# Performance work log

Measured on AMD Instinct MI355X. Metric: run time of the kernel, lower is better.

## Reference

```python
import jax, jax.numpy as jnp
import numpy as np

B, N, D = 8, 2048, 512

def setup_inputs() -> dict:
    key = jax.random.key(0)
    ks = jax.random.split(key, 8)
    s = 1.0 / np.sqrt(D)
    return {
        "inputs": jax.random.normal(ks[0], (B, N, D), dtype=jnp.float32),
        "mask": jnp.ones((B, N), dtype=jnp.int32),
        "Wk": jax.random.normal(ks[1], (D, D), dtype=jnp.float32) * s,
        "bk": jax.random.normal(ks[2], (D,), dtype=jnp.float32) * s,
        "Wq": jax.random.normal(ks[3], (D, D), dtype=jnp.float32) * s,
        "bq": jax.random.normal(ks[4], (D,), dtype=jnp.float32) * s,
        "Wv": jax.random.normal(ks[5], (D, D), dtype=jnp.float32) * s,
        "bv": jax.random.normal(ks[6], (D,), dtype=jnp.float32) * s,
    }

def reference(inputs, mask, Wk, bk, Wq, bq, Wv, bv):
    # torch Linear: y = x @ W.T + b
    keys = jnp.einsum('bnd,ed->bne', inputs, Wk) + bk
    queries = jnp.einsum('bnd,ed->bne', inputs, Wq) + bq
    values = jnp.einsum('bnd,ed->bne', inputs, Wv) + bv
    norm = jnp.sqrt(jnp.asarray(D, inputs.dtype))
    scores = jnp.einsum('bqd,bkd->bqk', queries, keys) / norm  # [B,N,N]
    scores = jnp.where(mask[:, None, :] == 0, jnp.asarray(-1e9, scores.dtype), scores)
    attn = jax.nn.softmax(scores, axis=-1)
    return jnp.einsum('bqk,bkd->bqd', attn, values)
```

## Files before the change

### kernel.cpp

```cpp
#include <hip/hip_runtime.h>
#include <hip/hip_bf16.h>


typedef __attribute__((ext_vector_type(8))) short short8;
typedef __attribute__((ext_vector_type(4))) float f32x4;

#define DEV __device__ __forceinline__
#define GLOBAL_AS __attribute__((address_space(1)))
#define LDS_AS __attribute__((address_space(3)))

static DEV ushort f2bs(float f) {
  union { float f; unsigned u; } x; x.f = f;
  unsigned r = (x.u + 0x7fffu + ((x.u >> 16) & 1u)) >> 16;
  return (ushort)r;
}

static DEV f32x4 mfma16(short8 a, short8 b, f32x4 c) {
  return __builtin_amdgcn_mfma_f32_16x16x32_bf16(a, b, c, 0, 0, 0);
}

static DEV void async16(const void* g, void* l) {
  __builtin_amdgcn_global_load_lds((const GLOBAL_AS void*)g, (LDS_AS void*)l, 16, 0, 0);
}

__global__ void convert_all(const float* __restrict__ wq, const float* __restrict__ wk,
                            const float* __restrict__ wv, const float* __restrict__ x,
                            ushort* __restrict__ wb, ushort* __restrict__ xb,
                            float* __restrict__ lde) {
  int i = blockIdx.x * 256 + threadIdx.x;
  if (i >= 2293760) {
    int off = (i - 2293760) * 4;
    float4 z; z.x = 0.f; z.y = 0.f; z.z = 0.f; z.w = 0.f;
    *(float4*)(lde + off) = z;
    return;
  }
  const float* src;
  ushort* dst;
  if (i < 196608) {
    int which = i >> 16;
    int off = (i & 65535) * 4;
    src = ((which == 0) ? wq : (which == 1) ? wk : wv) + off;
    dst = wb + (size_t)which * 262144 + off;
  } else {
    int off = (i - 196608) * 4;
    src = x + off;
    dst = xb + off;
  }
  float4 v = *(const float4*)src;
  ushort4 o;
  o.x = f2bs(v.x); o.y = f2bs(v.y); o.z = f2bs(v.z); o.w = f2bs(v.w);
  *(ushort4*)dst = o;
}

#define PH_ST_A(pp, kt, rd)                                                    \
  do {                                                                         \
    int rowbase_ = (rd) * 64 + wave * 8;                                       \
    int r_ = rowbase_ + (lane >> 3);                                           \
    int gc_ = (lane & 7) ^ (r_ & 7);                                           \
    async16(gA + (size_t)(arow0 + r_) * glda + (kt) * 64 + gc_ * 8,            \
            SdA + (pp) * 16384 + rowbase_ * 64);                               \
  } while (0)

#define PH_ST_B(pp, kt, rd)                                                    \
  do {                                                                         \
    int rowbase_ = (rd) * 64 + wave * 8;                                       \
    int r_ = rowbase_ + (lane >> 3);                                           \
    int gc_ = (lane & 7) ^ (r_ & 7);                                           \
    async16(gB + (size_t)(brow0 + r_) * gldb + (kt) * 64 + gc_ * 8,            \
            SdB + (pp) * 8192 + rowbase_ * 64);                                \
  } while (0)

#define PH_READ(pp, ks, afx, bfx)                                              \
  do {                                                                         \
    const ushort* Ap_ = SdA + (pp) * 16384;                                    \
    const ushort* Bp_ = SdB + (pp) * 8192;                                     \
    _Pragma("unroll")                                                          \
    for (int mf = 0; mf < 4; mf++) {                                           \
      int ra = wm * 64 + mf * 16 + c16;                                        \
      afx[mf] = *(const short8*)&Ap_[ra * 64 + ((((ks)*4 + quad) ^ (ra & 7)) * 8)]; \
    }                                                                          \
    _Pragma("unroll")                                                          \
    for (int nf = 0; nf < 4; nf++) {                                           \
      int rb = wn * 64 + nf * 16 + c16;                                        \
      bfx[nf] = *(const short8*)&Bp_[rb * 64 + ((((ks)*4 + quad) ^ (rb & 7)) * 8)]; \
    }                                                                          \
  } while (0)

#define PH_MFMA(afx, bfx, h)                                                   \
  do {                                                                         \
    __builtin_amdgcn_s_setprio(1);                                             \
    _Pragma("unroll")                                                          \
    for (int mf = (h) * 2; mf < (h) * 2 + 2; mf++)                             \
      _Pragma("unroll")                                                        \
      for (int nf = 0; nf < 4; nf++)                                           \
        acc[mf][nf] = mfma16(afx[mf], bfx[nf], acc[mf][nf]);                   \
    __builtin_amdgcn_s_setprio(0);                                             \
  } while (0)

#define PH_TILE(pp, kt, dostage)                                               \
  do {                                                                         \
    PH_READ(pp, 0, af0, bf0);                                                  \
    __builtin_amdgcn_s_barrier();                                              \
    asm volatile("s_waitcnt lgkmcnt(0)" ::: "memory");                         \
    __builtin_amdgcn_sched_barrier(0);                                         \
    PH_MFMA(af0, bf0, 0);                                                      \
    __builtin_amdgcn_s_barrier();                                              \
    PH_READ(pp, 1, af1, bf1);                                                  \
    __builtin_amdgcn_s_barrier();                                              \
    asm volatile("s_waitcnt lgkmcnt(0)" ::: "memory");                         \
    __builtin_amdgcn_sched_barrier(0);                                         \
    PH_MFMA(af0, bf0, 1);                                                      \
    __builtin_amdgcn_s_barrier();         \
    if (dostage) { PH_ST_A(pp, (kt) + 2, 0); PH_ST_A(pp, (kt) + 2, 1);         \
                   PH_ST_A(pp, (kt) + 2, 2); }                                 \
    PH_MFMA(af1, bf1, 0);                                                      \
    __builtin_amdgcn_s_barrier();                                              \
    if (dostage) { PH_ST_A(pp, (kt) + 2, 3); PH_ST_B(pp, (kt) + 2, 0);         \
                   PH_ST_B(pp, (kt) + 2, 1); }                                 \
    PH_MFMA(af1, bf1, 1);                                                      \
    if (dostage) { asm volatile("s_waitcnt vmcnt(6)" ::: "memory"); }          \
    else         { asm volatile("s_waitcnt vmcnt(0)" ::: "memory"); }          \
    __builtin_amdgcn_sched_barrier(0);                                         \
    __builtin_amdgcn_s_barrier();        \
  } while (0)

#define PH_PROLOGUE()                                                          \
  do {                                                                         \
    PH_ST_A(0, 0, 0); PH_ST_A(0, 0, 1); PH_ST_A(0, 0, 2); PH_ST_A(0, 0, 3);    \
    PH_ST_B(0, 0, 0); PH_ST_B(0, 0, 1);                                        \
    PH_ST_A(1, 1, 0); PH_ST_A(1, 1, 1); PH_ST_A(1, 1, 2); PH_ST_A(1, 1, 3);    \
    PH_ST_B(1, 1, 0); PH_ST_B(1, 1, 1);                                        \
    asm volatile("s_waitcnt vmcnt(6)" ::: "memory");                           \
    __builtin_amdgcn_sched_barrier(0);                                         \
    __builtin_amdgcn_s_barrier();                                              \
  } while (0)

__launch_bounds__(512, 2)
__global__ void qkv_gemm(const ushort* __restrict__ Xb, const ushort* __restrict__ Wb,
                         const float* __restrict__ bq, const float* __restrict__ bk,
                         const float* __restrict__ bv,
                         ushort* __restrict__ Qb, ushort* __restrict__ Kb,
                         ushort* __restrict__ Vtb) {
  const int rowblk = blockIdx.x;
  const int colblk = blockIdx.y;
  const int z = colblk >> 2;

  extern __shared__ ushort Sd[];
  ushort* SdA = Sd;
  ushort* SdB = Sd + 32768;

  const int tid = threadIdx.x;
  const int wave = tid >> 6, lane = tid & 63, quad = lane >> 4, c16 = lane & 15;
  const int wm = wave >> 1, wn = wave & 1;

  const ushort* gA = Xb;  const int glda = 512; const int arow0 = rowblk * 256;
  const ushort* gB = Wb;  const int gldb = 512; const int brow0 = colblk * 128;

  f32x4 acc[4][4];
#pragma unroll
  for (int mf = 0; mf < 4; mf++)
#pragma unroll
    for (int nf = 0; nf < 4; nf++) acc[mf][nf] = (f32x4)0.0f;

  PH_PROLOGUE();
  short8 af0[4], bf0[4], af1[4], bf1[4];
  for (int i = 0; i < 4; i++) {
    const int ds = (i < 3);
    PH_TILE(0, 2 * i, ds);
    PH_TILE(1, 2 * i + 1, ds);
  }

  const float* bias = (z == 0) ? bq : (z == 1) ? bk : bv;
  const int col0 = (colblk & 3) * 128 + wn * 64;
  float bvals[4];
#pragma unroll
  for (int nf = 0; nf < 4; nf++) bvals[nf] = bias[col0 + nf * 16 + c16];
  const float sc = (z == 0) ? 0.044194173824159216f : 1.0f;

  const int row0 = rowblk * 256 + wm * 64;
  if (z < 2) {
    ushort* O = (z == 0) ? Qb : Kb;
#pragma unroll
    for (int mf = 0; mf < 4; mf++)
#pragma unroll
      for (int nf = 0; nf < 4; nf++) {
        int el = col0 + nf * 16 + c16;
#pragma unroll
        for (int r = 0; r < 4; r++) {
          int n = row0 + mf * 16 + quad * 4 + r;
          O[(size_t)n * 512 + el] = f2bs((acc[mf][nf][r] + bvals[nf]) * sc);
        }
      }
  } else {
    __syncthreads();
    ushort* T = Sd;
#pragma unroll
    for (int nf = 0; nf < 4; nf++) {
      int ell = wn * 64 + nf * 16 + c16;
#pragma unroll
      for (int mf = 0; mf < 4; mf++) {
        int n0 = wm * 64 + mf * 16 + quad * 4;
        ushort4 o;
        o.x = f2bs(acc[mf][nf][0] + bvals[nf]);
        o.y = f2bs(acc[mf][nf][1] + bvals[nf]);
        o.z = f2bs(acc[mf][nf][2] + bvals[nf]);
        o.w = f2bs(acc[mf][nf][3] + bvals[nf]);
        *(ushort4*)&T[ell * 256 + (((n0 >> 3) ^ (ell & 31)) << 3) + (n0 & 4)] = o;
      }
    }
    __syncthreads();
    const int b = rowblk >> 3;
    const int nbase = (rowblk & 7) * 256;
    const int elbase = (colblk & 3) * 128;
    const int c4 = tid & 3, er = tid >> 2;
    size_t ge = ((size_t)b * 512 + elbase + er) * 2048;
#pragma unroll
    for (int j = 0; j < 8; j++) {
      int ch = j * 4 + c4;
      short8 v = *(short8*)&T[er * 256 + ((ch ^ (er & 31)) << 3)];
      *(short8*)(Vtb + ge + nbase + ch * 8) = v;
    }
  }
}

__launch_bounds__(512, 2)
__global__ void gemm_s(const ushort* __restrict__ Kb, const ushort* __restrict__ Qb,
                       const int* __restrict__ mask, ushort* __restrict__ Pm,
                       float* __restrict__ l) {
  const int bid = blockIdx.x;
  const int b = bid & 7;
  const int rowblk = (bid >> 3) & 7;
  const int colblk = bid >> 6;

  extern __shared__ ushort Sd[];
  ushort* SdA = Sd;
  ushort* SdB = Sd + 32768;

  const int tid = threadIdx.x;
  const int wave = tid >> 6, lane = tid & 63, quad = lane >> 4, c16 = lane & 15;
  const int wm = wave >> 1, wn = wave & 1;

  const ushort* gA = Kb + (size_t)b * 2048 * 512;  const int glda = 512;
  const int arow0 = rowblk * 256;
  const ushort* gB = Qb + (size_t)b * 2048 * 512;  const int gldb = 512;
  const int brow0 = colblk * 128;

  f32x4 acc[4][4];
#pragma unroll
  for (int mf = 0; mf < 4; mf++)
#pragma unroll
    for (int nf = 0; nf < 4; nf++) acc[mf][nf] = (f32x4)0.0f;

  PH_PROLOGUE();
  short8 af0[4], bf0[4], af1[4], bf1[4];
  for (int i = 0; i < 4; i++) {
    const int ds = (i < 3);
    PH_TILE(0, 2 * i, ds);
    PH_TILE(1, 2 * i + 1, ds);
  }

  float lpart[4] = {0.0f, 0.0f, 0.0f, 0.0f};
  __syncthreads();
  ushort* T = Sd;
#pragma unroll
  for (int mf = 0; mf < 4; mf++) {
    int keyl = wm * 64 + mf * 16 + quad * 4;
    int4 mv = *(const int4*)&mask[b * 2048 + rowblk * 256 + keyl];
    float m0 = mv.x ? 1.0f : 0.0f, m1 = mv.y ? 1.0f : 0.0f;
    float m2 = mv.z ? 1.0f : 0.0f, m3 = mv.w ? 1.0f : 0.0f;
#pragma unroll
    for (int nf = 0; nf < 4; nf++) {
      int ql = wn * 64 + nf * 16 + c16;
      float p0 = __expf(acc[mf][nf][0]) * m0;
      float p1 = __expf(acc[mf][nf][1]) * m1;
      float p2 = __expf(acc[mf][nf][2]) * m2;
      float p3 = __expf(acc[mf][nf][3]) * m3;
      ushort4 o;
      o.x = f2bs(p0); o.y = f2bs(p1); o.z = f2bs(p2); o.w = f2bs(p3);
      *(ushort4*)&T[ql * 256 + (((keyl >> 3) ^ (ql & 31)) << 3) + (keyl & 4)] = o;
      lpart[nf] += p0 + p1 + p2 + p3;
    }
  }
#pragma unroll
  for (int nf = 0; nf < 4; nf++) {
    float v = lpart[nf];
    v += __shfl_xor(v, 16, 64);
    v += __shfl_xor(v, 32, 64);
    if (quad == 0)
      atomicAdd(&l[b * 2048 + colblk * 128 + wn * 64 + nf * 16 + c16], v);
  }
  __syncthreads();
  {
    const int c4 = tid & 3, er = tid >> 2;
    size_t gq = ((size_t)b * 2048 + colblk * 128 + er) * 2048;
#pragma unroll
    for (int j = 0; j < 8; j++) {
      int ch = j * 4 + c4;
      short8 v = *(short8*)&T[er * 256 + ((ch ^ (er & 31)) << 3)];
      *(short8*)(Pm + gq + rowblk * 256 + ch * 8) = v;
    }
  }
}

__launch_bounds__(512, 2)
__global__ void gemm_o(const ushort* __restrict__ Pm, const ushort* __restrict__ Vtb,
                       const float* __restrict__ l, float* __restrict__ out) {
  const int bid = blockIdx.x;
  const int b = bid & 7;
  const int rowblk = (bid >> 3) & 7;
  const int colblk = bid >> 6;

  extern __shared__ ushort Sd[];
  ushort* SdA = Sd;
  ushort* SdB = Sd + 32768;

  const int tid = threadIdx.x;
  const int wave = tid >> 6, lane = tid & 63, quad = lane >> 4, c16 = lane & 15;
  const int wm = wave >> 1, wn = wave & 1;

  const ushort* gA = Pm + (size_t)b * 2048 * 2048;  const int glda = 2048;
  const int arow0 = rowblk * 256;
  const ushort* gB = Vtb + (size_t)b * 512 * 2048;  const int gldb = 2048;
  const int brow0 = colblk * 128;

  f32x4 acc[4][4];
#pragma unroll
  for (int mf = 0; mf < 4; mf++)
#pragma unroll
    for (int nf = 0; nf < 4; nf++) acc[mf][nf] = (f32x4)0.0f;

  PH_PROLOGUE();
  short8 af0[4], bf0[4], af1[4], bf1[4];
  for (int i = 0; i < 16; i++) {
    const int ds = (i < 15);
    PH_TILE(0, 2 * i, ds);
    PH_TILE(1, 2 * i + 1, ds);
  }

  const int row0 = rowblk * 256 + wm * 64;
  const int col0 = colblk * 128 + wn * 64;
  float linv[4][4];
#pragma unroll
  for (int mf = 0; mf < 4; mf++)
#pragma unroll
    for (int r = 0; r < 4; r++)
      linv[mf][r] = 1.0f / l[b * 2048 + row0 + mf * 16 + quad * 4 + r];
#pragma unroll
  for (int mf = 0; mf < 4; mf++)
#pragma unroll
    for (int nf = 0; nf < 4; nf++) {
      int col = col0 + nf * 16 + c16;
#pragma unroll
      for (int r = 0; r < 4; r++) {
        int row = row0 + mf * 16 + quad * 4 + r;
        out[((size_t)b * 2048 + row) * 512 + col] = acc[mf][nf][r] * linv[mf][r];
      }
    }
}

extern "C" void kernel_launch(void* const* d_in, const int* in_sizes, int n_in,
                              void* d_out, int out_size, void* d_ws, size_t ws_size,
                              hipStream_t stream) {
  (void)in_sizes; (void)n_in; (void)out_size; (void)ws_size;
  const float* X    = (const float*)d_in[0];
  const int*   mask = (const int*)d_in[1];
  const float* Wk   = (const float*)d_in[2];
  const float* bk   = (const float*)d_in[3];
  const float* Wq   = (const float*)d_in[4];
  const float* bq   = (const float*)d_in[5];
  const float* Wv   = (const float*)d_in[6];
  const float* bv   = (const float*)d_in[7];
  float* out = (float*)d_out;

  ushort* ws  = (ushort*)d_ws;
  ushort* Pm  = ws;
  ushort* Xb  = ws;
  ushort* Wb  = ws + (size_t)33554432;
  ushort* Qb  = Wb + (size_t)786432;
  ushort* Kb  = Qb + (size_t)8388608;
  ushort* Vtb = Kb + (size_t)8388608;
  float*  lde = (float*)(Vtb + (size_t)8388608);

  convert_all<<<8976, 256, 0, stream>>>(Wq, Wk, Wv, X, Wb, Xb, lde);
  qkv_gemm<<<dim3(64, 12), 512, 98304, stream>>>(Xb, Wb, bq, bk, bv, Qb, Kb, Vtb);
  gemm_s<<<1024, 512, 98304, stream>>>(Kb, Qb, mask, Pm, lde);
  gemm_o<<<256, 512, 98304, stream>>>(Pm, Vtb, lde, out);
}
```

Before: 218.8 us.

## Use single-buffered LDS GEMM loop in qkv and score kernels for higher occupancy

Replaces the double-buffered async-LDS pipelined mainloop in qkv_gemm and gemm_s with a simple single-buffer load/sync/compute step, halving LDS to 48KB and raising launch bounds to 4 blocks per CU. The transpose epilogues are split into two passes so they fit the smaller LDS. gemm_s also moves to a 3D grid with batch in z, which changes block scheduling order. The aim is to hide latency through more resident blocks instead of software pipelining. The cost is losing load/compute overlap within a block and adding barriers, and register pressure under the tighter launch bound may cause spills.

```diff
diff --git a/kernel.cpp b/kernel.cpp
--- a/kernel.cpp
+++ b/kernel.cpp
@@ -50,6 +50,216 @@
   ushort4 o;
   o.x = f2bs(v.x); o.y = f2bs(v.y); o.z = f2bs(v.z); o.w = f2bs(v.w);
   *(ushort4*)dst = o;
+}
+
+#define ST_A1(kt, rd)                                                          \
+  do {                                                                         \
+    int rowbase_ = (rd) * 64 + wave * 8;                                       \
+    int r_ = rowbase_ + (lane >> 3);                                           \
+    int gc_ = (lane & 7) ^ (r_ & 7);                                           \
+    async16(gA + (size_t)(arow0 + r_) * glda + (kt) * 64 + gc_ * 8,            \
+            SdA + rowbase_ * 64);                                              \
+  } while (0)
+
+#define ST_B1(kt, rd)                                                          \
+  do {                                                                         \
+    int rowbase_ = (rd) * 64 + wave * 8;                                       \
+    int r_ = rowbase_ + (lane >> 3);                                           \
+    int gc_ = (lane & 7) ^ (r_ & 7);                                           \
+    async16(gB + (size_t)(brow0 + r_) * gldb + (kt) * 64 + gc_ * 8,            \
+            SdB + rowbase_ * 64);                                              \
+  } while (0)
+
+#define SIMPLE_STEP(kt)                                                        \
+  do {                                                                         \
+    __syncthreads();                                                           \
+    ST_A1(kt, 0); ST_A1(kt, 1); ST_A1(kt, 2); ST_A1(kt, 3);                    \
+    ST_B1(kt, 0); ST_B1(kt, 1);                                                \
+    __syncthreads();                                                           \
+    _Pragma("unroll")                                                          \
+    for (int ks = 0; ks < 2; ks++) {                                           \
+      short8 af[4], bf[4];                                                     \
+      _Pragma("unroll")                                                        \
+      for (int mf = 0; mf < 4; mf++) {                                         \
+        int ra = wm * 64 + mf * 16 + c16;                                      \
+        af[mf] = *(const short8*)&SdA[ra * 64 + (((ks * 4 + quad) ^ (ra & 7)) * 8)]; \
+      }                                                                        \
+      _Pragma("unroll")                                                        \
+      for (int nf = 0; nf < 4; nf++) {                                         \
+        int rb = wn * 64 + nf * 16 + c16;                                      \
+        bf[nf] = *(const short8*)&SdB[rb * 64 + (((ks * 4 + quad) ^ (rb & 7)) * 8)]; \
+      }                                                                        \
+      _Pragma("unroll")                                                        \
+      for (int mf = 0; mf < 4; mf++)                                           \
+        _Pragma("unroll")                                                      \
+        for (int nf = 0; nf < 4; nf++)                                         \
+          acc[mf][nf] = mfma16(af[mf], bf[nf], acc[mf][nf]);                   \
+    }                                                                          \
+  } while (0)
+
+__launch_bounds__(512, 4)
+__global__ void qkv_gemm(const ushort* __restrict__ Xb, const ushort* __restrict__ Wb,
+                         const float* __restrict__ bq, const float* __restrict__ bk,
+                         const float* __restrict__ bv,
+                         ushort* __restrict__ Qb, ushort* __restrict__ Kb,
+                         ushort* __restrict__ Vtb) {
+  const int rowblk = blockIdx.x;
+  const int colblk = blockIdx.y;
+  const int z = colblk >> 2;
+
+  extern __shared__ ushort Sd[];
+  ushort* SdA = Sd;
+  ushort* SdB = Sd + 16384;
+
+  const int tid = threadIdx.x;
+  const int wave = tid >> 6, lane = tid & 63, quad = lane >> 4, c16 = lane & 15;
+  const int wm = wave >> 1, wn = wave & 1;
+
+  const ushort* gA = Xb;  const int glda = 512; const int arow0 = rowblk * 256;
+  const ushort* gB = Wb;  const int gldb = 512; const int brow0 = colblk * 128;
+
+  f32x4 acc[4][4];
+#pragma unroll
+  for (int mf = 0; mf < 4; mf++)
+#pragma unroll
+    for (int nf = 0; nf < 4; nf++) acc[mf][nf] = (f32x4)0.0f;
+
+  for (int kt = 0; kt < 8; kt++) SIMPLE_STEP(kt);
+
+  const float* bias = (z == 0) ? bq : (z == 1) ? bk : bv;
+  const int col0 = (colblk & 3) * 128 + wn * 64;
+  float bvals[4];
+#pragma unroll
+  for (int nf = 0; nf < 4; nf++) bvals[nf] = bias[col0 + nf * 16 + c16];
+  const float sc = (z == 0) ? 0.044194173824159216f : 1.0f;
+
+  const int row0 = rowblk * 256 + wm * 64;
+  if (z < 2) {
+    ushort* O = (z == 0) ? Qb : Kb;
+#pragma unroll
+    for (int mf = 0; mf < 4; mf++)
+#pragma unroll
+      for (int nf = 0; nf < 4; nf++) {
+        int el = col0 + nf * 16 + c16;
+#pragma unroll
+        for (int r = 0; r < 4; r++) {
+          int n = row0 + mf * 16 + quad * 4 + r;
+          O[(size_t)n * 512 + el] = f2bs((acc[mf][nf][r] + bvals[nf]) * sc);
+        }
+      }
+  } else {
+    ushort* T = Sd;
+    const int bb = rowblk >> 3;
+    const int nbase = (rowblk & 7) * 256;
+    const int elbase = (colblk & 3) * 128;
+    const int c4 = tid & 3, er = tid >> 2;
+    __syncthreads();
+#pragma unroll
+    for (int pass = 0; pass < 2; pass++) {
+      if ((wm >> 1) == pass) {
+#pragma unroll
+        for (int nf = 0; nf < 4; nf++) {
+          int ell = wn * 64 + nf * 16 + c16;
+#pragma unroll
+          for (int mf = 0; mf < 4; mf++) {
+            int n0p = (wm & 1) * 64 + mf * 16 + quad * 4;
+            ushort4 o;
+            o.x = f2bs(acc[mf][nf][0] + bvals[nf]);
+            o.y = f2bs(acc[mf][nf][1] + bvals[nf]);
+            o.z = f2bs(acc[mf][nf][2] + bvals[nf]);
+            o.w = f2bs(acc[mf][nf][3] + bvals[nf]);
+            *(ushort4*)&T[ell * 128 + (((n0p >> 3) ^ (ell & 15)) << 3) + (n0p & 4)] = o;
+          }
+        }
+      }
+      __syncthreads();
+      size_t ge = ((size_t)bb * 512 + elbase + er) * 2048;
+#pragma unroll
+      for (int j = 0; j < 4; j++) {
+        int ch = j * 4 + c4;
+        short8 v = *(short8*)&T[er * 128 + ((ch ^ (er & 15)) << 3)];
+        *(short8*)(Vtb + ge + nbase + pass * 128 + ch * 8) = v;
+      }
+      __syncthreads();
+    }
+  }
+}
+
+__launch_bounds__(512, 4)
+__global__ void gemm_s(const ushort* __restrict__ Kb, const ushort* __restrict__ Qb,
+                       const int* __restrict__ mask, ushort* __restrict__ Pm,
+                       float* __restrict__ l) {
+  const int b = blockIdx.z;
+  const int rowblk = blockIdx.x;
+  const int colblk = blockIdx.y;
+
+  extern __shared__ ushort Sd[];
+  ushort* SdA = Sd;
+  ushort* SdB = Sd + 16384;
+
+  const int tid = threadIdx.x;
+  const int wave = tid >> 6, lane = tid & 63, quad = lane >> 4, c16 = lane & 15;
+  const int wm = wave >> 1, wn = wave & 1;
+
+  const ushort* gA = Kb + (size_t)b * 2048 * 512;  const int glda = 512;
+  const int arow0 = rowblk * 256;
+  const ushort* gB = Qb + (size_t)b * 2048 * 512;  const int gldb = 512;
+  const int brow0 = colblk * 128;
+
+  f32x4 acc[4][4];
+#pragma unroll
+  for (int mf = 0; mf < 4; mf++)
+#pragma unroll
+    for (int nf = 0; nf < 4; nf++) acc[mf][nf] = (f32x4)0.0f;
+
+  for (int kt = 0; kt < 8; kt++) SIMPLE_STEP(kt);
+
+  float lpart[4] = {0.0f, 0.0f, 0.0f, 0.0f};
+  ushort* T = Sd;
+  const int c4 = tid & 3, er = tid >> 2;
+  __syncthreads();
+#pragma unroll
+  for (int pass = 0; pass < 2; pass++) {
+    if ((wm >> 1) == pass) {
+#pragma unroll
+      for (int mf = 0; mf < 4; mf++) {
+        int k0p = (wm & 1) * 64 + mf * 16 + quad * 4;
+        int keyg = rowblk * 256 + pass * 128 + k0p;
+        int4 mv = *(const int4*)&mask[b * 2048 + keyg];
+        float m0 = mv.x ? 1.0f : 0.0f, m1 = mv.y ? 1.0f : 0.0f;
+        float m2 = mv.z ? 1.0f : 0.0f, m3 = mv.w ? 1.0f : 0.0f;
+#pragma unroll
+        for (int nf = 0; nf < 4; nf++) {
+          int ql = wn * 64 + nf * 16 + c16;
+          float p0 = __expf(acc[mf][nf][0]) * m0;
+          float p1 = __expf(acc[mf][nf][1]) * m1;
+          float p2 = __expf(acc[mf][nf][2]) * m2;
+          float p3 = __expf(acc[mf][nf][3]) * m3;
+          ushort4 o;
+          o.x = f2bs(p0); o.y = f2bs(p1); o.z = f2bs(p2); o.w = f2bs(p3);
+          *(ushort4*)&T[ql * 128 + (((k0p >> 3) ^ (ql & 15)) << 3) + (k0p & 4)] = o;
+          lpart[nf] += p0 + p1 + p2 + p3;
+        }
+      }
+    }
+    __syncthreads();
+    size_t gq = ((size_t)b * 2048 + colblk * 128 + er) * 2048;
+#pragma unroll
+    for (int j = 0; j < 4; j++) {
+      int ch = j * 4 + c4;
+      short8 v = *(short8*)&T[er * 128 + ((ch ^ (er & 15)) << 3)];
+      *(short8*)(Pm + gq + rowblk * 256 + pass * 128 + ch * 8) = v;
+    }
+    __syncthreads();
+  }
+#pragma unroll
+  for (int nf = 0; nf < 4; nf++) {
+    float v = lpart[nf];
+    v += __shfl_xor(v, 16, 64);
+    v += __shfl_xor(v, 32, 64);
+    if (quad == 0)
+      atomicAdd(&l[b * 2048 + colblk * 128 + wn * 64 + nf * 16 + c16], v);
+  }
 }
 
 #define PH_ST_A(pp, kt, rd)                                                    \
@@ -136,173 +346,6 @@
   } while (0)
 
 __launch_bounds__(512, 2)
-__global__ void qkv_gemm(const ushort* __restrict__ Xb, const ushort* __restrict__ Wb,
-                         const float* __restrict__ bq, const float* __restrict__ bk,
-                         const float* __restrict__ bv,
-                         ushort* __restrict__ Qb, ushort* __restrict__ Kb,
-                         ushort* __restrict__ Vtb) {
-  const int rowblk = blockIdx.x;
-  const int colblk = blockIdx.y;
-  const int z = colblk >> 2;
-
-  extern __shared__ ushort Sd[];
-  ushort* SdA = Sd;
-  ushort* SdB = Sd + 32768;
-
-  const int tid = threadIdx.x;
-  const int wave = tid >> 6, lane = tid & 63, quad = lane >> 4, c16 = lane & 15;
-  const int wm = wave >> 1, wn = wave & 1;
-
-  const ushort* gA = Xb;  const int glda = 512; const int arow0 = rowblk * 256;
-  const ushort* gB = Wb;  const int gldb = 512; const int brow0 = colblk * 128;
-
-  f32x4 acc[4][4];
-#pragma unroll
-  for (int mf = 0; mf < 4; mf++)
-#pragma unroll
-    for (int nf = 0; nf < 4; nf++) acc[mf][nf] = (f32x4)0.0f;
-
-  PH_PROLOGUE();
-  short8 af0[4], bf0[4], af1[4], bf1[4];
-  for (int i = 0; i < 4; i++) {
-    const int ds = (i < 3);
-    PH_TILE(0, 2 * i, ds);
-    PH_TILE(1, 2 * i + 1, ds);
-  }
-
-  const float* bias = (z == 0) ? bq : (z == 1) ? bk : bv;
-  const int col0 = (colblk & 3) * 128 + wn * 64;
-  float bvals[4];
-#pragma unroll
-  for (int nf = 0; nf < 4; nf++) bvals[nf] = bias[col0 + nf * 16 + c16];
-  const float sc = (z == 0) ? 0.044194173824159216f : 1.0f;
-
-  const int row0 = rowblk * 256 + wm * 64;
-  if (z < 2) {
-    ushort* O = (z == 0) ? Qb : Kb;
-#pragma unroll
-    for (int mf = 0; mf < 4; mf++)
-#pragma unroll
-      for (int nf = 0; nf < 4; nf++) {
-        int el = col0 + nf * 16 + c16;
-#pragma unroll
-        for (int r = 0; r < 4; r++) {
-          int n = row0 + mf * 16 + quad * 4 + r;
-          O[(size_t)n * 512 + el] = f2bs((acc[mf][nf][r] + bvals[nf]) * sc);
-        }
-      }
-  } else {
-    __syncthreads();
-    ushort* T = Sd;
-#pragma unroll
-    for (int nf = 0; nf < 4; nf++) {
-      int ell = wn * 64 + nf * 16 + c16;
-#pragma unroll
-      for (int mf = 0; mf < 4; mf++) {
-        int n0 = wm * 64 + mf * 16 + quad * 4;
-        ushort4 o;
-        o.x = f2bs(acc[mf][nf][0] + bvals[nf]);
-        o.y = f2bs(acc[mf][nf][1] + bvals[nf]);
-        o.z = f2bs(acc[mf][nf][2] + bvals[nf]);
-        o.w = f2bs(acc[mf][nf][3] + bvals[nf]);
-        *(ushort4*)&T[ell * 256 + (((n0 >> 3) ^ (ell & 31)) << 3) + (n0 & 4)] = o;
-      }
-    }
-    __syncthreads();
-    const int b = rowblk >> 3;
-    const int nbase = (rowblk & 7) * 256;
-    const int elbase = (colblk & 3) * 128;
-    const int c4 = tid & 3, er = tid >> 2;
-    size_t ge = ((size_t)b * 512 + elbase + er) * 2048;
-#pragma unroll
-    for (int j = 0; j < 8; j++) {
-      int ch = j * 4 + c4;
-      short8 v = *(short8*)&T[er * 256 + ((ch ^ (er & 31)) << 3)];
-      *(short8*)(Vtb + ge + nbase + ch * 8) = v;
-    }
-  }
-}
-
-__launch_bounds__(512, 2)
-__global__ void gemm_s(const ushort* __restrict__ Kb, const ushort* __restrict__ Qb,
-                       const int* __restrict__ mask, ushort* __restrict__ Pm,
-                       float* __restrict__ l) {
-  const int bid = blockIdx.x;
-  const int b = bid & 7;
-  const int rowblk = (bid >> 3) & 7;
-  const int colblk = bid >> 6;
-
-  extern __shared__ ushort Sd[];
-  ushort* SdA = Sd;
-  ushort* SdB = Sd + 32768;
-
-  const int tid = threadIdx.x;
-  const int wave = tid >> 6, lane = tid & 63, quad = lane >> 4, c16 = lane & 15;
-  const int wm = wave >> 1, wn = wave & 1;
-
-  const ushort* gA = Kb + (size_t)b * 2048 * 512;  const int glda = 512;
-  const int arow0 = rowblk * 256;
-  const ushort* gB = Qb + (size_t)b * 2048 * 512;  const int gldb = 512;
-  const int brow0 = colblk * 128;
-
-  f32x4 acc[4][4];
-#pragma unroll
-  for (int mf = 0; mf < 4; mf++)
-#pragma unroll
-    for (int nf = 0; nf < 4; nf++) acc[mf][nf] = (f32x4)0.0f;
-
-  PH_PROLOGUE();
-  short8 af0[4], bf0[4], af1[4], bf1[4];
-  for (int i = 0; i < 4; i++) {
-    const int ds = (i < 3);
-    PH_TILE(0, 2 * i, ds);
-    PH_TILE(1, 2 * i + 1, ds);
-  }
-
-  float lpart[4] = {0.0f, 0.0f, 0.0f, 0.0f};
-  __syncthreads();
-  ushort* T = Sd;
-#pragma unroll
-  for (int mf = 0; mf < 4; mf++) {
-    int keyl = wm * 64 + mf * 16 + quad * 4;
-    int4 mv = *(const int4*)&mask[b * 2048 + rowblk * 256 + keyl];
-    float m0 = mv.x ? 1.0f : 0.0f, m1 = mv.y ? 1.0f : 0.0f;
-    float m2 = mv.z ? 1.0f : 0.0f, m3 = mv.w ? 1.0f : 0.0f;
-#pragma unroll
-    for (int nf = 0; nf < 4; nf++) {
-      int ql = wn * 64 + nf * 16 + c16;
-      float p0 = __expf(acc[mf][nf][0]) * m0;
-      float p1 = __expf(acc[mf][nf][1]) * m1;
-      float p2 = __expf(acc[mf][nf][2]) * m2;
-      float p3 = __expf(acc[mf][nf][3]) * m3;
-      ushort4 o;
-      o.x = f2bs(p0); o.y = f2bs(p1); o.z = f2bs(p2); o.w = f2bs(p3);
-      *(ushort4*)&T[ql * 256 + (((keyl >> 3) ^ (ql & 31)) << 3) + (keyl & 4)] = o;
-      lpart[nf] += p0 + p1 + p2 + p3;
-    }
-  }
-#pragma unroll
-  for (int nf = 0; nf < 4; nf++) {
-    float v = lpart[nf];
-    v += __shfl_xor(v, 16, 64);
-    v += __shfl_xor(v, 32, 64);
-    if (quad == 0)
-      atomicAdd(&l[b * 2048 + colblk * 128 + wn * 64 + nf * 16 + c16], v);
-  }
-  __syncthreads();
-  {
-    const int c4 = tid & 3, er = tid >> 2;
-    size_t gq = ((size_t)b * 2048 + colblk * 128 + er) * 2048;
-#pragma unroll
-    for (int j = 0; j < 8; j++) {
-      int ch = j * 4 + c4;
-      short8 v = *(short8*)&T[er * 256 + ((ch ^ (er & 31)) << 3)];
-      *(short8*)(Pm + gq + rowblk * 256 + ch * 8) = v;
-    }
-  }
-}
-
-__launch_bounds__(512, 2)
 __global__ void gemm_o(const ushort* __restrict__ Pm, const ushort* __restrict__ Vtb,
                        const float* __restrict__ l, float* __restrict__ out) {
   const int bid = blockIdx.x;
@@ -382,7 +425,7 @@
   float*  lde = (float*)(Vtb + (size_t)8388608);
 
   convert_all<<<8976, 256, 0, stream>>>(Wq, Wk, Wv, X, Wb, Xb, lde);
-  qkv_gemm<<<dim3(64, 12), 512, 98304, stream>>>(Xb, Wb, bq, bk, bv, Qb, Kb, Vtb);
-  gemm_s<<<1024, 512, 98304, stream>>>(Kb, Qb, mask, Pm, lde);
+  qkv_gemm<<<dim3(64, 12), 512, 49152, stream>>>(Xb, Wb, bq, bk, bv, Qb, Kb, Vtb);
+  gemm_s<<<dim3(8, 16, 8), 512, 49152, stream>>>(Kb, Qb, mask, Pm, lde);
   gemm_o<<<256, 512, 98304, stream>>>(Pm, Vtb, lde, out);
 }
```

New measurement: 220.7 us. No clear change (+0.9%).
